# Optimization experiments

Hardware: AMD Instinct MI355X
Metric: run time of the kernel (lower is better)

The kernel has to match this reference:

```python
import jax, jax.numpy as jnp
import numpy as np

DIM = 1024
NUM_HEADS = 16
HEAD_DIM = DIM // NUM_HEADS


def setup_inputs() -> dict:
    key = jax.random.key(0)
    k_x, k_wqkv, k_bqkv, k_wo, k_bo = jax.random.split(key, 5)
    scale = DIM ** -0.5
    return {
        "x": jax.random.normal(k_x, (4, 2048, DIM), dtype=jnp.float32),
        "w_qkv": jax.random.normal(k_wqkv, (DIM, 3 * DIM), dtype=jnp.float32) * scale,
        "b_qkv": jax.random.normal(k_bqkv, (3 * DIM,), dtype=jnp.float32) * 0.02,
        "w_out": jax.random.normal(k_wo, (DIM, DIM), dtype=jnp.float32) * scale,
        "b_out": jax.random.normal(k_bo, (DIM,), dtype=jnp.float32) * 0.02,
    }


def reference(x, w_qkv, b_qkv, w_out, b_out):
    B, S, D = x.shape
    H, Hd = NUM_HEADS, HEAD_DIM
    # QKV projection: (B,S,3D) -> (3,B,H,S,Hd)
    qkv = (x @ w_qkv + b_qkv).reshape(B, S, 3, H, Hd).transpose(2, 0, 3, 1, 4)
    q, k, v = qkv[0], qkv[1], qkv[2]
    scores = jnp.einsum('bhqd,bhkd->bhqk', q, k) / (Hd ** 0.5)
    attn = jax.nn.softmax(scores, axis=-1)  # dropout is identity in eval
    out = jnp.einsum('bhqk,bhkd->bhqd', attn, v)
    out = out.transpose(0, 2, 1, 3).reshape(B, S, D)
    return out @ w_out + b_out
```

## Files before the change

### kernel.cpp

```cpp
#include <hip/hip_runtime.h>
#include <hip/hip_bf16.h>
#include <stdint.h>

#define SEQ 2048
#define DIM 1024
#define NH 16
#define HD 64

typedef __attribute__((ext_vector_type(8))) short short8;
typedef __attribute__((ext_vector_type(4))) float f32x4;
typedef __attribute__((ext_vector_type(4))) float float4v;
typedef __attribute__((ext_vector_type(4))) unsigned short u16x4;
typedef __attribute__((ext_vector_type(2))) unsigned int u32x2;

#define MFMA16(a, b, c) __builtin_amdgcn_mfma_f32_16x16x32_bf16(a, b, c, 0, 0, 0)

#define QSCALE 0.1803368801111244f
#define LOG2_THR 11.0f

__device__ __forceinline__ unsigned short f2b(float f) {
  union { float f; unsigned int u; } x; x.f = f;
  unsigned int r = (x.u + 0x7FFFu + ((x.u >> 16) & 1u)) >> 16;
  return (unsigned short)r;
}

__device__ __forceinline__ unsigned int pk2(float a, float b) {
  __hip_bfloat162 h = __float22bfloat162_rn(float2{a, b});
  union { __hip_bfloat162 h; unsigned int u; } c; c.h = h;
  return c.u;
}

__device__ __forceinline__ void gld16(const void* g, void* l) {
  __builtin_amdgcn_global_load_lds(
      (const __attribute__((address_space(1))) unsigned int*)(uintptr_t)g,
      (__attribute__((address_space(3))) unsigned int*)(unsigned int)(uintptr_t)l,
      16, 0, 0);
}

__global__ void cast_bf16_kernel(const float* __restrict__ in,
                                 unsigned short* __restrict__ out, int n4) {
  int stride = gridDim.x * blockDim.x;
  for (int i = blockIdx.x * blockDim.x + threadIdx.x; i < n4; i += stride) {
    float4v v = *(const float4v*)(in + (size_t)i * 4);
    u16x4 o;
    o.x = f2b(v.x); o.y = f2b(v.y); o.z = f2b(v.z); o.w = f2b(v.w);
    *(u16x4*)(out + (size_t)i * 4) = o;
  }
}

__global__ void transpose_cast_kernel(const float* __restrict__ in,
                                      unsigned short* __restrict__ out,
                                      int rows, int cols) {
  __shared__ float tile[32][33];
  const int t = threadIdx.x, tx = t & 31, ty = t >> 5;
  const int c0 = blockIdx.x * 32, r0 = blockIdx.y * 32;
#pragma unroll
  for (int j = 0; j < 4; j++)
    tile[ty + 8 * j][tx] = in[(size_t)(r0 + ty + 8 * j) * cols + c0 + tx];
  __syncthreads();
#pragma unroll
  for (int j = 0; j < 4; j++)
    out[(size_t)(c0 + ty + 8 * j) * rows + r0 + tx] = f2b(tile[tx][ty + 8 * j]);
}

template <int EPI>
__global__ __launch_bounds__(256, 2) void gemm_bt_kernel(
    const unsigned short* __restrict__ A, const unsigned short* __restrict__ Bt,
    const float* __restrict__ bias, float* __restrict__ Cf,
    int M, int N, int K,
    unsigned short* __restrict__ Qb, unsigned short* __restrict__ Kb,
    unsigned short* __restrict__ Vt) {
  __shared__ unsigned short lA[128 * 32];
  __shared__ unsigned short lB[128 * 32];
  const int t = threadIdx.x, lane = t & 63, w = t >> 6;
  const int l15 = lane & 15, lg = lane >> 4;
  const int wr = (w >> 1) * 64, wc = (w & 1) * 64;
  const int bm = blockIdx.x, bn = blockIdx.y;
  const char* Ag = (const char*)(A + (size_t)bm * 128 * K);
  const char* Bg = (const char*)(Bt + (size_t)bn * 128 * K);
  const int sr = t >> 2;
  const int sc = (t & 3) * 16;
  const size_t rowb = (size_t)K * 2;

  f32x4 acc[4][4];
#pragma unroll
  for (int m = 0; m < 4; m++)
#pragma unroll
    for (int n = 0; n < 4; n++) acc[m][n] = (f32x4){0.f, 0.f, 0.f, 0.f};

  for (int k0 = 0; k0 < K; k0 += 32) {
    __syncthreads();
    const size_t kbyte = (size_t)k0 * 2;
    gld16(Ag + (size_t)sr * rowb + kbyte + sc, &lA[t * 8]);
    gld16(Ag + (size_t)(sr + 64) * rowb + kbyte + sc, &lA[2048 + t * 8]);
    gld16(Bg + (size_t)sr * rowb + kbyte + sc, &lB[t * 8]);
    gld16(Bg + (size_t)(sr + 64) * rowb + kbyte + sc, &lB[2048 + t * 8]);
    asm volatile("s_waitcnt vmcnt(0)" ::: "memory");
    __syncthreads();
    short8 af[4], bf_[4];
#pragma unroll
    for (int m = 0; m < 4; m++)
      af[m] = *(const short8*)&lA[(wr + m * 16 + l15) * 32 + lg * 8];
#pragma unroll
    for (int n = 0; n < 4; n++)
      bf_[n] = *(const short8*)&lB[(wc + n * 16 + l15) * 32 + lg * 8];
#pragma unroll
    for (int m = 0; m < 4; m++)
#pragma unroll
      for (int n = 0; n < 4; n++)
        acc[m][n] = MFMA16(af[m], bf_[n], acc[m][n]);
  }

#pragma unroll
  for (int m = 0; m < 4; m++) {
#pragma unroll
    for (int n = 0; n < 4; n++) {
      const int row0 = bm * 128 + wr + m * 16 + lg * 4;
      const int col = bn * 128 + wc + n * 16 + l15;
      const float bv = bias[col];
#pragma unroll
      for (int rr = 0; rr < 4; rr++) {
        const float v = acc[m][n][rr] + bv;
        const int row = row0 + rr;
        if (EPI == 1) {
          Cf[(size_t)row * N + col] = v;
        } else {
          const int three = col >> 10, rem = col & 1023;
          const int h = rem >> 6, d = rem & 63;
          const int b = row >> 11, s = row & 2047;
          const size_t bh = (size_t)(b * NH + h);
          if (three == 0)
            Qb[(bh * SEQ + s) * HD + d] = f2b(v * QSCALE);
          else if (three == 1)
            Kb[(bh * SEQ + s) * HD + d] = f2b(v);
          else
            Vt[(bh * HD + d) * SEQ + s] = f2b(v);
        }
      }
    }
  }
}

__global__ __launch_bounds__(256, 3) void attn_kernel(
    const unsigned short* __restrict__ Qb, const unsigned short* __restrict__ Kb,
    const unsigned short* __restrict__ Vt, unsigned short* __restrict__ AO) {
  __shared__ unsigned short kT[2][64 * 64];
  __shared__ unsigned short vT[2][64 * 64];
  __shared__ unsigned short pT[4][32 * 64];
  const int t = threadIdx.x, lane = t & 63, w = t >> 6;
  const int l15 = lane & 15, lg = lane >> 4;
  const int q0 = blockIdx.x * 128;
  const int bh = blockIdx.y;
  const char* Qg = (const char*)(Qb + (size_t)bh * SEQ * HD);
  const char* Kg = (const char*)(Kb + (size_t)bh * SEQ * HD);
  const char* Vg = (const char*)(Vt + (size_t)bh * HD * SEQ);

  short8 qa[2][2];
#pragma unroll
  for (int h = 0; h < 2; h++) {
    const char* qrow = Qg + (size_t)(q0 + w * 32 + h * 16 + l15) * 128;
    qa[h][0] = *(const short8*)(qrow + lg * 16);
    qa[h][1] = *(const short8*)(qrow + 64 + lg * 16);
  }

  f32x4 o[2][4];
#pragma unroll
  for (int h = 0; h < 2; h++)
#pragma unroll
    for (int n = 0; n < 4; n++) o[h][n] = (f32x4){0.f, 0.f, 0.f, 0.f};
  float m_r[2] = {-1e30f, -1e30f}, l_r[2] = {0.f, 0.f};

  const int sr0 = t >> 3;
  const int scx = (t & 7) * 16;

#define STAGE(buf, kv0_)                                                               \
  do {                                                                                 \
    const int r0_ = sr0, r1_ = sr0 + 32;                                               \
    gld16(Kg + (size_t)((kv0_) + r0_) * 128 + (scx ^ ((r0_ & 7) << 4)),                \
          &kT[buf][t * 8]);                                                            \
    gld16(Kg + (size_t)((kv0_) + r1_) * 128 + (scx ^ ((r1_ & 7) << 4)),                \
          &kT[buf][2048 + t * 8]);                                                     \
    gld16(Vg + (size_t)r0_ * (SEQ * 2) + (size_t)(kv0_) * 2 + (scx ^ ((r0_ & 7) << 4)),\
          &vT[buf][t * 8]);                                                            \
    gld16(Vg + (size_t)r1_ * (SEQ * 2) + (size_t)(kv0_) * 2 + (scx ^ ((r1_ & 7) << 4)),\
          &vT[buf][2048 + t * 8]);                                                     \
  } while (0)

  STAGE(0, 0);
  asm volatile("s_waitcnt vmcnt(0)" ::: "memory");
  __syncthreads();
  int cur = 0;

  for (int kv0 = 0; kv0 < SEQ; kv0 += 64) {
    if (kv0 + 64 < SEQ) STAGE(cur ^ 1, kv0 + 64);

    const char* kb = (const char*)&kT[cur][0];
    f32x4 s[2][4];
#pragma unroll
    for (int h = 0; h < 2; h++)
#pragma unroll
      for (int n = 0; n < 4; n++) s[h][n] = (f32x4){0.f, 0.f, 0.f, 0.f};
    __builtin_amdgcn_s_setprio(1);
#pragma unroll
    for (int n = 0; n < 4; n++) {
      const int row = n * 16 + l15;
      const char* kr = kb + row * 128;
      const int sw = (row & 7) << 4;
      short8 a0 = *(const short8*)(kr + ((lg * 16) ^ sw));
      short8 a1 = *(const short8*)(kr + ((64 + lg * 16) ^ sw));
      s[0][n] = MFMA16(a0, qa[0][0], s[0][n]);
      s[0][n] = MFMA16(a1, qa[0][1], s[0][n]);
      s[1][n] = MFMA16(a0, qa[1][0], s[1][n]);
      s[1][n] = MFMA16(a1, qa[1][1], s[1][n]);
    }
    __builtin_amdgcn_s_setprio(0);

    float mx[2];
#pragma unroll
    for (int h = 0; h < 2; h++) {
      float m0 = fmaxf(fmaxf(s[h][0][0], s[h][0][1]), fmaxf(s[h][0][2], s[h][0][3]));
#pragma unroll
      for (int n = 1; n < 4; n++) {
        m0 = fmaxf(m0, fmaxf(fmaxf(s[h][n][0], s[h][n][1]), fmaxf(s[h][n][2], s[h][n][3])));
      }
      m0 = fmaxf(m0, __shfl_xor(m0, 16, 64));
      m0 = fmaxf(m0, __shfl_xor(m0, 32, 64));
      mx[h] = m0;
    }

    const int grow = (mx[0] > m_r[0] + LOG2_THR) | (mx[1] > m_r[1] + LOG2_THR);
    if (__any(grow)) {
      float al[2];
#pragma unroll
      for (int h = 0; h < 2; h++) {
        const float nm = fmaxf(m_r[h], mx[h]);
        al[h] = exp2f(m_r[h] - nm);
        m_r[h] = nm;
        l_r[h] *= al[h];
      }
#pragma unroll
      for (int h = 0; h < 2; h++)
#pragma unroll
        for (int r = 0; r < 4; r++) {
          const float alb = __shfl(al[h], lg * 4 + r, 64);
#pragma unroll
          for (int n = 0; n < 4; n++) o[h][n][r] *= alb;
        }
    }

    char* pb = (char*)&pT[w][0];
    const int swp = (l15 & 7) << 4;
#pragma unroll
    for (int h = 0; h < 2; h++) {
      float rs = 0.f;
#pragma unroll
      for (int n = 0; n < 4; n++) {
#pragma unroll
        for (int r = 0; r < 4; r++) {
          const float p = exp2f(s[h][n][r] - m_r[h]);
          s[h][n][r] = p;
          rs += p;
        }
        u32x2 c;
        c.x = pk2(s[h][n][0], s[h][n][1]);
        c.y = pk2(s[h][n][2], s[h][n][3]);
        *(u32x2*)(pb + (h * 16 + l15) * 128 + ((n * 32 + lg * 8) ^ swp)) = c;
      }
      rs += __shfl_xor(rs, 16, 64);
      rs += __shfl_xor(rs, 32, 64);
      l_r[h] += rs;
    }
    short8 pa[2][2];
#pragma unroll
    for (int h = 0; h < 2; h++) {
      const char* pr = pb + (h * 16 + l15) * 128;
      pa[h][0] = *(const short8*)(pr + ((lg * 16) ^ swp));
      pa[h][1] = *(const short8*)(pr + ((64 + lg * 16) ^ swp));
    }

    const char* vb = (const char*)&vT[cur][0];
    __builtin_amdgcn_s_setprio(1);
#pragma unroll
    for (int n = 0; n < 4; n++) {
      const int row = n * 16 + l15;
      const char* vr = vb + row * 128;
      const int sw = (row & 7) << 4;
      short8 b0 = *(const short8*)(vr + ((lg * 16) ^ sw));
      short8 b1 = *(const short8*)(vr + ((64 + lg * 16) ^ sw));
      o[0][n] = MFMA16(pa[0][0], b0, o[0][n]);
      o[0][n] = MFMA16(pa[0][1], b1, o[0][n]);
      o[1][n] = MFMA16(pa[1][0], b0, o[1][n]);
      o[1][n] = MFMA16(pa[1][1], b1, o[1][n]);
    }
    __builtin_amdgcn_s_setprio(0);

    asm volatile("s_waitcnt vmcnt(0)" ::: "memory");
    __syncthreads();
    cur ^= 1;
  }
#undef STAGE

  float inv[2];
#pragma unroll
  for (int h = 0; h < 2; h++) inv[h] = 1.f / l_r[h];
  const int b = bh >> 4, hh = bh & 15;
  unsigned short* aob = AO + (size_t)b * SEQ * DIM + (size_t)hh * HD;
#pragma unroll
  for (int h = 0; h < 2; h++)
#pragma unroll
    for (int r = 0; r < 4; r++) {
      const float lb = __shfl(inv[h], lg * 4 + r, 64);
      const int s_ = q0 + w * 32 + h * 16 + lg * 4 + r;
#pragma unroll
      for (int n = 0; n < 4; n++) {
        const int d_ = n * 16 + l15;
        aob[(size_t)s_ * DIM + d_] = f2b(o[h][n][r] * lb);
      }
    }
}

extern "C" void kernel_launch(void* const* d_in, const int* in_sizes, int n_in,
                              void* d_out, int out_size, void* d_ws, size_t ws_size,
                              hipStream_t stream) {
  const float* x = (const float*)d_in[0];
  const float* w_qkv = (const float*)d_in[1];
  const float* b_qkv = (const float*)d_in[2];
  const float* w_out = (const float*)d_in[3];
  const float* b_out = (const float*)d_in[4];
  float* out = (float*)d_out;

  char* ws = (char*)d_ws;
  unsigned short* xb    = (unsigned short*)(ws);
  unsigned short* wqkvT = (unsigned short*)(ws + (16u << 20));
  unsigned short* woT   = (unsigned short*)(ws + (22u << 20));
  unsigned short* Qb    = (unsigned short*)(ws + (24u << 20));
  unsigned short* Kb    = (unsigned short*)(ws + (40u << 20));
  unsigned short* Vt    = (unsigned short*)(ws + (56u << 20));
  unsigned short* AO    = (unsigned short*)(ws + (72u << 20));

  const int M = 4 * SEQ;

  cast_bf16_kernel<<<2048, 256, 0, stream>>>(x, xb, M * DIM / 4);
  transpose_cast_kernel<<<dim3(3 * DIM / 32, DIM / 32), 256, 0, stream>>>(w_qkv, wqkvT, DIM, 3 * DIM);
  transpose_cast_kernel<<<dim3(DIM / 32, DIM / 32), 256, 0, stream>>>(w_out, woT, DIM, DIM);

  gemm_bt_kernel<0><<<dim3(M / 128, 3 * DIM / 128), 256, 0, stream>>>(
      xb, wqkvT, b_qkv, nullptr, M, 3 * DIM, DIM, Qb, Kb, Vt);

  attn_kernel<<<dim3(SEQ / 128, 4 * NH), 256, 0, stream>>>(Qb, Kb, Vt, AO);

  gemm_bt_kernel<1><<<dim3(M / 128, DIM / 128), 256, 0, stream>>>(
      AO, woT, b_out, out, M, DIM, DIM, nullptr, nullptr, nullptr);
}
```

Baseline: 329.8 us.

## Use 128-key attention tiles, XCD-aware block remap, and vectorized V-transpose stores

The attention kernel now processes 128 keys per iteration instead of 64, so it runs half as many barrier and wait steps and computes one running max per 128 keys. Blocks are remapped so that all query tiles of one head run on the same XCD, which is meant to improve L2 reuse of that head's K and V. The QKV epilogue now writes the transposed V with 4-element vector stores and hoists the index math out of the row loop. The cost is double the LDS for K and V, which lowers occupancy (launch bounds drop from 3 to 2 blocks), and more score registers per thread.

Measured after the change: 324.8 us. No clear change (-1.5%).

```diff
diff --git a/kernel.cpp b/kernel.cpp
--- a/kernel.cpp
+++ b/kernel.cpp
@@ -118,39 +118,46 @@
       const int row0 = bm * 128 + wr + m * 16 + lg * 4;
       const int col = bn * 128 + wc + n * 16 + l15;
       const float bv = bias[col];
-#pragma unroll
-      for (int rr = 0; rr < 4; rr++) {
-        const float v = acc[m][n][rr] + bv;
-        const int row = row0 + rr;
-        if (EPI == 1) {
-          Cf[(size_t)row * N + col] = v;
+      if (EPI == 1) {
+#pragma unroll
+        for (int rr = 0; rr < 4; rr++)
+          Cf[(size_t)(row0 + rr) * N + col] = acc[m][n][rr] + bv;
+      } else {
+        const int three = col >> 10, rem = col & 1023;
+        const int h = rem >> 6, d = rem & 63;
+        const int b = row0 >> 11, s0 = row0 & 2047;
+        const size_t bh = (size_t)(b * NH + h);
+        if (three == 0) {
+#pragma unroll
+          for (int rr = 0; rr < 4; rr++)
+            Qb[(bh * SEQ + s0 + rr) * HD + d] = f2b((acc[m][n][rr] + bv) * QSCALE);
+        } else if (three == 1) {
+#pragma unroll
+          for (int rr = 0; rr < 4; rr++)
+            Kb[(bh * SEQ + s0 + rr) * HD + d] = f2b(acc[m][n][rr] + bv);
         } else {
-          const int three = col >> 10, rem = col & 1023;
-          const int h = rem >> 6, d = rem & 63;
-          const int b = row >> 11, s = row & 2047;
-          const size_t bh = (size_t)(b * NH + h);
-          if (three == 0)
-            Qb[(bh * SEQ + s) * HD + d] = f2b(v * QSCALE);
-          else if (three == 1)
-            Kb[(bh * SEQ + s) * HD + d] = f2b(v);
-          else
-            Vt[(bh * HD + d) * SEQ + s] = f2b(v);
+          u16x4 pk;
+#pragma unroll
+          for (int rr = 0; rr < 4; rr++) pk[rr] = f2b(acc[m][n][rr] + bv);
+          *(u16x4*)&Vt[(bh * HD + d) * SEQ + s0] = pk;
         }
       }
     }
   }
 }
 
-__global__ __launch_bounds__(256, 3) void attn_kernel(
+__global__ __launch_bounds__(256, 2) void attn_kernel(
     const unsigned short* __restrict__ Qb, const unsigned short* __restrict__ Kb,
     const unsigned short* __restrict__ Vt, unsigned short* __restrict__ AO) {
-  __shared__ unsigned short kT[2][64 * 64];
-  __shared__ unsigned short vT[2][64 * 64];
+  __shared__ unsigned short kT[2][128 * 64];
+  __shared__ unsigned short vT[2][64 * 128];
   __shared__ unsigned short pT[4][32 * 64];
   const int t = threadIdx.x, lane = t & 63, w = t >> 6;
   const int l15 = lane & 15, lg = lane >> 4;
-  const int q0 = blockIdx.x * 128;
-  const int bh = blockIdx.y;
+  const int flat = blockIdx.y * 16 + blockIdx.x;
+  const int xcd = flat & 7, j = flat >> 3;
+  const int bh = xcd * 8 + (j >> 4);
+  const int q0 = (j & 15) * 128;
   const char* Qg = (const char*)(Qb + (size_t)bh * SEQ * HD);
   const char* Kg = (const char*)(Kb + (size_t)bh * SEQ * HD);
   const char* Vg = (const char*)(Vt + (size_t)bh * HD * SEQ);
@@ -170,59 +177,68 @@
     for (int n = 0; n < 4; n++) o[h][n] = (f32x4){0.f, 0.f, 0.f, 0.f};
   float m_r[2] = {-1e30f, -1e30f}, l_r[2] = {0.f, 0.f};
 
-  const int sr0 = t >> 3;
-  const int scx = (t & 7) * 16;
-
-#define STAGE(buf, kv0_)                                                               \
-  do {                                                                                 \
-    const int r0_ = sr0, r1_ = sr0 + 32;                                               \
-    gld16(Kg + (size_t)((kv0_) + r0_) * 128 + (scx ^ ((r0_ & 7) << 4)),                \
-          &kT[buf][t * 8]);                                                            \
-    gld16(Kg + (size_t)((kv0_) + r1_) * 128 + (scx ^ ((r1_ & 7) << 4)),                \
-          &kT[buf][2048 + t * 8]);                                                     \
-    gld16(Vg + (size_t)r0_ * (SEQ * 2) + (size_t)(kv0_) * 2 + (scx ^ ((r0_ & 7) << 4)),\
-          &vT[buf][t * 8]);                                                            \
-    gld16(Vg + (size_t)r1_ * (SEQ * 2) + (size_t)(kv0_) * 2 + (scx ^ ((r1_ & 7) << 4)),\
-          &vT[buf][2048 + t * 8]);                                                     \
+#define STAGE2(buf, kv0_)                                                          \
+  do {                                                                             \
+    _Pragma("unroll")                                                              \
+    for (int i_ = 0; i_ < 4; i_++) {                                               \
+      const int kr_ = i_ * 32 + (t >> 3);                                          \
+      const int kc_ = (t & 7) * 16;                                                \
+      gld16(Kg + (size_t)((kv0_) + kr_) * 128 + (kc_ ^ ((kr_ & 7) << 4)),          \
+            &kT[buf][i_ * 2048 + t * 8]);                                          \
+    }                                                                              \
+    _Pragma("unroll")                                                              \
+    for (int i_ = 0; i_ < 4; i_++) {                                               \
+      const int vd_ = i_ * 16 + (t >> 4);                                          \
+      const int vc_ = (t & 15) * 16;                                               \
+      gld16(Vg + (size_t)vd_ * (SEQ * 2) + (size_t)(kv0_) * 2 +                    \
+                (vc_ ^ ((vd_ & 7) << 4)),                                          \
+            &vT[buf][i_ * 2048 + t * 8]);                                          \
+    }                                                                              \
   } while (0)
 
-  STAGE(0, 0);
+  STAGE2(0, 0);
   asm volatile("s_waitcnt vmcnt(0)" ::: "memory");
   __syncthreads();
   int cur = 0;
 
-  for (int kv0 = 0; kv0 < SEQ; kv0 += 64) {
-    if (kv0 + 64 < SEQ) STAGE(cur ^ 1, kv0 + 64);
+  for (int kv0 = 0; kv0 < SEQ; kv0 += 128) {
+    if (kv0 + 128 < SEQ) STAGE2(cur ^ 1, kv0 + 128);
 
     const char* kb = (const char*)&kT[cur][0];
-    f32x4 s[2][4];
-#pragma unroll
-    for (int h = 0; h < 2; h++)
-#pragma unroll
-      for (int n = 0; n < 4; n++) s[h][n] = (f32x4){0.f, 0.f, 0.f, 0.f};
+    f32x4 s[2][2][4];
+#pragma unroll
+    for (int tau = 0; tau < 2; tau++)
+#pragma unroll
+      for (int h = 0; h < 2; h++)
+#pragma unroll
+        for (int n = 0; n < 4; n++) s[tau][h][n] = (f32x4){0.f, 0.f, 0.f, 0.f};
     __builtin_amdgcn_s_setprio(1);
 #pragma unroll
-    for (int n = 0; n < 4; n++) {
-      const int row = n * 16 + l15;
-      const char* kr = kb + row * 128;
-      const int sw = (row & 7) << 4;
-      short8 a0 = *(const short8*)(kr + ((lg * 16) ^ sw));
-      short8 a1 = *(const short8*)(kr + ((64 + lg * 16) ^ sw));
-      s[0][n] = MFMA16(a0, qa[0][0], s[0][n]);
-      s[0][n] = MFMA16(a1, qa[0][1], s[0][n]);
-      s[1][n] = MFMA16(a0, qa[1][0], s[1][n]);
-      s[1][n] = MFMA16(a1, qa[1][1], s[1][n]);
-    }
+    for (int tau = 0; tau < 2; tau++)
+#pragma unroll
+      for (int n = 0; n < 4; n++) {
+        const int row = tau * 64 + n * 16 + l15;
+        const char* kr = kb + row * 128;
+        const int sw = (row & 7) << 4;
+        short8 a0 = *(const short8*)(kr + ((lg * 16) ^ sw));
+        short8 a1 = *(const short8*)(kr + ((64 + lg * 16) ^ sw));
+        s[tau][0][n] = MFMA16(a0, qa[0][0], s[tau][0][n]);
+        s[tau][0][n] = MFMA16(a1, qa[0][1], s[tau][0][n]);
+        s[tau][1][n] = MFMA16(a0, qa[1][0], s[tau][1][n]);
+        s[tau][1][n] = MFMA16(a1, qa[1][1], s[tau][1][n]);
+      }
     __builtin_amdgcn_s_setprio(0);
 
     float mx[2];
 #pragma unroll
     for (int h = 0; h < 2; h++) {
-      float m0 = fmaxf(fmaxf(s[h][0][0], s[h][0][1]), fmaxf(s[h][0][2], s[h][0][3]));
-#pragma unroll
-      for (int n = 1; n < 4; n++) {
-        m0 = fmaxf(m0, fmaxf(fmaxf(s[h][n][0], s[h][n][1]), fmaxf(s[h][n][2], s[h][n][3])));
-      }
+      float m0 = s[0][h][0][0];
+#pragma unroll
+      for (int tau = 0; tau < 2; tau++)
+#pragma unroll
+        for (int n = 0; n < 4; n++)
+#pragma unroll
+          for (int r = 0; r < 4; r++) m0 = fmaxf(m0, s[tau][h][n][r]);
       m0 = fmaxf(m0, __shfl_xor(m0, 16, 64));
       m0 = fmaxf(m0, __shfl_xor(m0, 32, 64));
       mx[h] = m0;
@@ -248,57 +264,62 @@
         }
     }
 
+    float rs[2] = {0.f, 0.f};
     char* pb = (char*)&pT[w][0];
     const int swp = (l15 & 7) << 4;
-#pragma unroll
-    for (int h = 0; h < 2; h++) {
-      float rs = 0.f;
+    const char* vb = (const char*)&vT[cur][0];
+#pragma unroll
+    for (int tau = 0; tau < 2; tau++) {
+#pragma unroll
+      for (int h = 0; h < 2; h++) {
+#pragma unroll
+        for (int n = 0; n < 4; n++) {
+#pragma unroll
+          for (int r = 0; r < 4; r++) {
+            const float p = exp2f(s[tau][h][n][r] - m_r[h]);
+            s[tau][h][n][r] = p;
+            rs[h] += p;
+          }
+          u32x2 c;
+          c.x = pk2(s[tau][h][n][0], s[tau][h][n][1]);
+          c.y = pk2(s[tau][h][n][2], s[tau][h][n][3]);
+          *(u32x2*)(pb + (h * 16 + l15) * 128 + ((n * 32 + lg * 8) ^ swp)) = c;
+        }
+      }
+      short8 pa[2][2];
+#pragma unroll
+      for (int h = 0; h < 2; h++) {
+        const char* pr = pb + (h * 16 + l15) * 128;
+        pa[h][0] = *(const short8*)(pr + ((lg * 16) ^ swp));
+        pa[h][1] = *(const short8*)(pr + ((64 + lg * 16) ^ swp));
+      }
+      __builtin_amdgcn_s_setprio(1);
 #pragma unroll
       for (int n = 0; n < 4; n++) {
-#pragma unroll
-        for (int r = 0; r < 4; r++) {
-          const float p = exp2f(s[h][n][r] - m_r[h]);
-          s[h][n][r] = p;
-          rs += p;
-        }
-        u32x2 c;
-        c.x = pk2(s[h][n][0], s[h][n][1]);
-        c.y = pk2(s[h][n][2], s[h][n][3]);
-        *(u32x2*)(pb + (h * 16 + l15) * 128 + ((n * 32 + lg * 8) ^ swp)) = c;
-      }
-      rs += __shfl_xor(rs, 16, 64);
-      rs += __shfl_xor(rs, 32, 64);
-      l_r[h] += rs;
-    }
-    short8 pa[2][2];
-#pragma unroll
-    for (int h = 0; h < 2; h++) {
-      const char* pr = pb + (h * 16 + l15) * 128;
-      pa[h][0] = *(const short8*)(pr + ((lg * 16) ^ swp));
-      pa[h][1] = *(const short8*)(pr + ((64 + lg * 16) ^ swp));
-    }
-
-    const char* vb = (const char*)&vT[cur][0];
-    __builtin_amdgcn_s_setprio(1);
-#pragma unroll
-    for (int n = 0; n < 4; n++) {
-      const int row = n * 16 + l15;
-      const char* vr = vb + row * 128;
-      const int sw = (row & 7) << 4;
-      short8 b0 = *(const short8*)(vr + ((lg * 16) ^ sw));
-      short8 b1 = *(const short8*)(vr + ((64 + lg * 16) ^ sw));
-      o[0][n] = MFMA16(pa[0][0], b0, o[0][n]);
-      o[0][n] = MFMA16(pa[0][1], b1, o[0][n]);
-      o[1][n] = MFMA16(pa[1][0], b0, o[1][n]);
-      o[1][n] = MFMA16(pa[1][1], b1, o[1][n]);
-    }
-    __builtin_amdgcn_s_setprio(0);
+        const int row = n * 16 + l15;
+        const char* vr = vb + row * 256;
+        const int sw = (row & 7) << 4;
+        short8 b0 = *(const short8*)(vr + ((tau * 128 + lg * 16) ^ sw));
+        short8 b1 = *(const short8*)(vr + ((tau * 128 + 64 + lg * 16) ^ sw));
+        o[0][n] = MFMA16(pa[0][0], b0, o[0][n]);
+        o[0][n] = MFMA16(pa[0][1], b1, o[0][n]);
+        o[1][n] = MFMA16(pa[1][0], b0, o[1][n]);
+        o[1][n] = MFMA16(pa[1][1], b1, o[1][n]);
+      }
+      __builtin_amdgcn_s_setprio(0);
+    }
+    rs[0] += __shfl_xor(rs[0], 16, 64);
+    rs[0] += __shfl_xor(rs[0], 32, 64);
+    rs[1] += __shfl_xor(rs[1], 16, 64);
+    rs[1] += __shfl_xor(rs[1], 32, 64);
+    l_r[0] += rs[0];
+    l_r[1] += rs[1];
 
     asm volatile("s_waitcnt vmcnt(0)" ::: "memory");
     __syncthreads();
     cur ^= 1;
   }
-#undef STAGE
+#undef STAGE2
 
   float inv[2];
 #pragma unroll
```
